# Kernel tuning notes

Hardware: AMD Instinct MI355X
Metric: run time of the kernel (lower is better)

## Reference

```python
import jax, jax.numpy as jnp
import numpy as np

NEG = -1e30  # stand-in for -inf on the H-attention diagonal (matches INF helper)


def _conv1x1(w, b, x):
    # w: [O, C], x: [B, C, H, W]
    return jnp.einsum('oc,bchw->bohw', w, x) + b[None, :, None, None]


def _cc_attn(q, k, v):
    """Criss-cross attention: q,k [B,Cq,H,W], v [B,C,H,W] -> [B,C,H,W]."""
    B, _, H, W = q.shape
    # column (H) energies: query at (h,w) attends to keys at (h', w)
    eH = jnp.einsum('bchw,bcjw->bhwj', q, k)  # [B,H,W,H]
    eye = jnp.eye(H, dtype=bool)[None, :, None, :]
    eH = jnp.where(eye, NEG, eH)  # mask h==h' (self counted once via W pass)
    # row (W) energies: query at (h,w) attends to keys at (h, w')
    eW = jnp.einsum('bchw,bchj->bhwj', q, k)  # [B,H,W,W]
    att = jax.nn.softmax(jnp.concatenate([eH, eW], axis=3), axis=3)  # [B,H,W,H+W]
    aH, aW = att[..., :H], att[..., H:]
    outH = jnp.einsum('bhwj,bcjw->bchw', aH, v)
    outW = jnp.einsum('bhwj,bchj->bchw', aW, v)
    return outH + outW


def setup_inputs() -> dict:
    key = jax.random.key(0)
    ks = jax.random.split(key, 14)
    B, C, H, W = 8, 256, 96, 96
    Cq = C // 8
    n = jax.random.normal
    return {
        'x': n(ks[0], (B, C, H, W), jnp.float32),
        'y': n(ks[1], (B, C, H, W), jnp.float32),
        'Wq': n(ks[2], (Cq, C), jnp.float32) * 0.05,
        'bq': n(ks[3], (Cq,), jnp.float32) * 0.05,
        'Wk': n(ks[4], (Cq, C), jnp.float32) * 0.05,
        'bk': n(ks[5], (Cq,), jnp.float32) * 0.05,
        'Wv': n(ks[6], (C, C), jnp.float32) * 0.05,
        'bv': n(ks[7], (C,), jnp.float32) * 0.05,
        'gamma1': n(ks[8], (1,), jnp.float32) * 0.1,
        'gamma2': n(ks[9], (1,), jnp.float32) * 0.1,
        'Wd': n(ks[10], (2 * C, 1, 3, 3), jnp.float32) * 0.1,  # depthwise, groups=2C
        'bd': n(ks[11], (2 * C,), jnp.float32) * 0.05,
        'Wp': n(ks[12], (C, 2 * C), jnp.float32) * 0.05,  # pointwise 1x1
        'bp': n(ks[13], (C,), jnp.float32) * 0.05,
    }


def reference(x, y, Wq, bq, Wk, bk, Wv, bv, gamma1, gamma2, Wd, bd, Wp, bp):
    qx = _conv1x1(Wq, bq, x)
    kx = _conv1x1(Wk, bk, x)
    vx = _conv1x1(Wv, bv, x)
    qy = _conv1x1(Wq, bq, y)
    ky = _conv1x1(Wk, bk, y)
    vy = _conv1x1(Wv, bv, y)
    # pass 1: attention weights from x, values from y
    out1 = gamma1[0] * _cc_attn(qx, kx, vy) + x
    # pass 2: attention weights from y, values from x
    out2 = gamma2[0] * _cc_attn(qy, ky, vx) + y
    z = jnp.concatenate([out1, out2], axis=1)  # [B, 2C, H, W]
    # depthwise 3x3 (groups = 2C), padding 1
    z = jax.lax.conv_general_dilated(
        z, Wd, window_strides=(1, 1), padding='SAME',
        feature_group_count=z.shape[1],
        dimension_numbers=('NCHW', 'OIHW', 'NCHW')) + bd[None, :, None, None]
    # pointwise 1x1 then LeakyReLU (torch default negative_slope=0.01)
    z = _conv1x1(Wp, bp, z)
    return jax.nn.leaky_relu(z, negative_slope=0.01)
```

## Files before the change

kernel.cpp:

```cpp
#include <hip/hip_runtime.h>
#include <hip/hip_bf16.h>

constexpr int kB  = 8;
constexpr int kC  = 256;
constexpr int kCq = 32;
constexpr int kH  = 96;
constexpr int kW  = 96;
constexpr int kP  = kH * kW;

using bf16x8 = __attribute__((ext_vector_type(8))) short;
using bf16x4 = __attribute__((ext_vector_type(4))) short;
using f32x4  = __attribute__((ext_vector_type(4))) float;

__device__ inline bf16x8 ld_lds8(const __hip_bfloat16* p) {
    bf16x4 lo = *(const bf16x4*)p;
    bf16x4 hi = *(const bf16x4*)(p + 4);
    return __builtin_shufflevector(lo, hi, 0, 1, 2, 3, 4, 5, 6, 7);
}

__global__ __launch_bounds__(256) void w_convert(
    const float* __restrict__ Wq, const float* __restrict__ Wk,
    const float* __restrict__ Wv,
    __hip_bfloat16* __restrict__ Wqkb, __hip_bfloat16* __restrict__ Wvb)
{
    const int i = blockIdx.x * 256 + threadIdx.x;
    if (i < 8192)       Wqkb[i] = __float2bfloat16(Wq[i]);
    else if (i < 16384) Wqkb[i] = __float2bfloat16(Wk[i - 8192]);
    else                Wvb[i - 16384] = __float2bfloat16(Wv[i - 16384]);
}

__global__ __launch_bounds__(256, 2) void qkv_mfma(
    const float* __restrict__ in_qk, const float* __restrict__ in_v,
    const __hip_bfloat16* __restrict__ Wqkb, const __hip_bfloat16* __restrict__ Wvb,
    const float* __restrict__ bq, const float* __restrict__ bk,
    const float* __restrict__ bv,
    __hip_bfloat16* __restrict__ Qbh, __hip_bfloat16* __restrict__ Qbl,
    __hip_bfloat16* __restrict__ Kbh, __hip_bfloat16* __restrict__ Kbl,
    __hip_bfloat16* __restrict__ Vpm, __hip_bfloat16* __restrict__ Vhw)
{
    __shared__ __align__(16) char smem[34816];
    __hip_bfloat16* sqb = (__hip_bfloat16*)smem;
    __hip_bfloat16* svb = sqb + 2 * 64 * 36;
    __hip_bfloat16* vt  = (__hip_bfloat16*)smem;

    const int b = blockIdx.y, t = threadIdx.x;
    const int wv = t >> 6, l = t & 63;
    const int n = l & 15, q = l >> 4;
    const int p0 = blockIdx.x * 64;
    const int p  = p0 + wv * 16 + n;
    const size_t bP = (size_t)b * kP;

    const float* __restrict__ xq = in_qk + (size_t)b * kC * kP + p0;
    const float* __restrict__ xv = in_v  + (size_t)b * kC * kP + p0;

    const int sc = t >> 4;
    const int sp = (t & 15) * 4;

    f32x4 acc[20];
#pragma unroll
    for (int i = 0; i < 20; i++) acc[i] = (f32x4)0.f;

    {
        float4 q0 = *(const float4*)&xq[(size_t)sc * kP + sp];
        float4 q1 = *(const float4*)&xq[(size_t)(16 + sc) * kP + sp];
        float4 v0 = *(const float4*)&xv[(size_t)sc * kP + sp];
        float4 v1 = *(const float4*)&xv[(size_t)(16 + sc) * kP + sp];
        float fq0[4] = { q0.x, q0.y, q0.z, q0.w };
        float fq1[4] = { q1.x, q1.y, q1.z, q1.w };
        float fv0[4] = { v0.x, v0.y, v0.z, v0.w };
        float fv1[4] = { v1.x, v1.y, v1.z, v1.w };
#pragma unroll
        for (int j = 0; j < 4; j++) {
            sqb[(sp + j) * 36 + sc]      = __float2bfloat16(fq0[j]);
            sqb[(sp + j) * 36 + 16 + sc] = __float2bfloat16(fq1[j]);
            svb[(sp + j) * 36 + sc]      = __float2bfloat16(fv0[j]);
            svb[(sp + j) * 36 + 16 + sc] = __float2bfloat16(fv1[j]);
        }
    }
    __syncthreads();

    int cur = 0;
    for (int kc = 0; kc < 8; kc++) {
        float4 nq0, nq1, nv0, nv1;
        if (kc < 7) {
            const size_t cb = (size_t)(kc + 1) * 32;
            nq0 = *(const float4*)&xq[(cb + sc) * kP + sp];
            nq1 = *(const float4*)&xq[(cb + 16 + sc) * kP + sp];
            nv0 = *(const float4*)&xv[(cb + sc) * kP + sp];
            nv1 = *(const float4*)&xv[(cb + 16 + sc) * kP + sp];
        }

        const int c0 = kc * 32 + q * 8;

        bf16x8 wq[4], wv2[16];
#pragma unroll
        for (int mt = 0; mt < 4; mt++)
            wq[mt] = *(const bf16x8*)(Wqkb + ((mt * 16 + n) << 8) + c0);
#pragma unroll
        for (int mt = 0; mt < 16; mt++)
            wv2[mt] = *(const bf16x8*)(Wvb + ((mt * 16 + n) << 8) + c0);

        const __hip_bfloat16* sqp = sqb + cur * 2304 + (wv * 16 + n) * 36 + q * 8;
        const __hip_bfloat16* svp = svb + cur * 2304 + (wv * 16 + n) * 36 + q * 8;
        bf16x8 bfq = ld_lds8(sqp);
        bf16x8 bfv = ld_lds8(svp);

#pragma unroll
        for (int mt = 0; mt < 4; mt++)
            acc[mt] = __builtin_amdgcn_mfma_f32_16x16x32_bf16(wq[mt], bfq, acc[mt], 0, 0, 0);
#pragma unroll
        for (int mt = 0; mt < 16; mt++)
            acc[4 + mt] = __builtin_amdgcn_mfma_f32_16x16x32_bf16(wv2[mt], bfv, acc[4 + mt], 0, 0, 0);

        if (kc < 7) {
            const int nb = cur ^ 1;
            __hip_bfloat16* dq = sqb + nb * 2304;
            __hip_bfloat16* dv = svb + nb * 2304;
            float fq0[4] = { nq0.x, nq0.y, nq0.z, nq0.w };
            float fq1[4] = { nq1.x, nq1.y, nq1.z, nq1.w };
            float fv0[4] = { nv0.x, nv0.y, nv0.z, nv0.w };
            float fv1[4] = { nv1.x, nv1.y, nv1.z, nv1.w };
#pragma unroll
            for (int j = 0; j < 4; j++) {
                dq[(sp + j) * 36 + sc]      = __float2bfloat16(fq0[j]);
                dq[(sp + j) * 36 + 16 + sc] = __float2bfloat16(fq1[j]);
                dv[(sp + j) * 36 + sc]      = __float2bfloat16(fv0[j]);
                dv[(sp + j) * 36 + 16 + sc] = __float2bfloat16(fv1[j]);
            }
        }
        __syncthreads();
        cur ^= 1;
    }

#pragma unroll
    for (int mt = 0; mt < 2; mt++) {
        float4 bias = *(const float4*)&bq[mt * 16 + q * 4];
        float vv[4] = { acc[mt][0] + bias.x, acc[mt][1] + bias.y,
                        acc[mt][2] + bias.z, acc[mt][3] + bias.w };
        union { ushort4 u; __hip_bfloat16 h[4]; } hi, lo;
#pragma unroll
        for (int r = 0; r < 4; r++) {
            __hip_bfloat16 h = __float2bfloat16(vv[r]);
            hi.h[r] = h;
            lo.h[r] = __float2bfloat16(vv[r] - __bfloat162float(h));
        }
        *(ushort4*)&Qbh[(bP + p) * kCq + mt * 16 + q * 4] = hi.u;
        *(ushort4*)&Qbl[(bP + p) * kCq + mt * 16 + q * 4] = lo.u;
    }
#pragma unroll
    for (int mt = 2; mt < 4; mt++) {
        float4 bias = *(const float4*)&bk[(mt - 2) * 16 + q * 4];
        float vv[4] = { acc[mt][0] + bias.x, acc[mt][1] + bias.y,
                        acc[mt][2] + bias.z, acc[mt][3] + bias.w };
        union { ushort4 u; __hip_bfloat16 h[4]; } hi, lo;
#pragma unroll
        for (int r = 0; r < 4; r++) {
            __hip_bfloat16 h = __float2bfloat16(vv[r]);
            hi.h[r] = h;
            lo.h[r] = __float2bfloat16(vv[r] - __bfloat162float(h));
        }
        *(ushort4*)&Kbh[(bP + p) * kCq + (mt - 2) * 16 + q * 4] = hi.u;
        *(ushort4*)&Kbl[(bP + p) * kCq + (mt - 2) * 16 + q * 4] = lo.u;
    }

#pragma unroll
    for (int mt = 0; mt < 16; mt++) {
        float4 bias = *(const float4*)&bv[mt * 16 + q * 4];
        float vv[4] = { acc[4 + mt][0] + bias.x, acc[4 + mt][1] + bias.y,
                        acc[4 + mt][2] + bias.z, acc[4 + mt][3] + bias.w };
        union { ushort4 u; __hip_bfloat16 h[4]; } pm;
#pragma unroll
        for (int r = 0; r < 4; r++) pm.h[r] = __float2bfloat16(vv[r]);
        *(ushort4*)&Vpm[(bP + p) * kC + mt * 16 + q * 4] = pm.u;
#pragma unroll
        for (int r = 0; r < 4; r++)
            vt[(mt * 16 + q * 4 + r) * 68 + wv * 16 + n] = pm.h[r];
    }
    __syncthreads();

    {
        __hip_bfloat16* dst = Vhw + ((size_t)b * kC + t) * kP + p0;
#pragma unroll
        for (int j = 0; j < 8; j++) {
            bf16x8 row = ld_lds8(&vt[t * 68 + j * 8]);
            *(bf16x8*)&dst[j * 8] = row;
        }
    }
}

__global__ __launch_bounds__(256) void cc_stats(
    const __hip_bfloat16* __restrict__ Qbh, const __hip_bfloat16* __restrict__ Qbl,
    const __hip_bfloat16* __restrict__ Kbh, const __hip_bfloat16* __restrict__ Kbl,
    float* __restrict__ Sm, float* __restrict__ Si)
{
    __shared__ __align__(16) __hip_bfloat16 QH[96][36], QLo[96][36];
    __shared__ __align__(16) __hip_bfloat16 KH[96][36], KLo[96][36];
    __shared__ __align__(16) float EL[96][97];
    const int w = blockIdx.x, b = blockIdx.y;
    const int t = threadIdx.x;
    const size_t bP = (size_t)b * kP;

    for (int idx = t; idx < 768; idx += 256) {
        int row = idx >> 3, ch = (idx & 7) * 4;
        size_t g = (bP + (size_t)row * kW + w) * kCq + ch;
        *(ushort4*)&QH[row][ch]  = *(const ushort4*)&Qbh[g];
        *(ushort4*)&QLo[row][ch] = *(const ushort4*)&Qbl[g];
        *(ushort4*)&KH[row][ch]  = *(const ushort4*)&Kbh[g];
        *(ushort4*)&KLo[row][ch] = *(const ushort4*)&Kbl[g];
    }
    __syncthreads();

    const int wv = t >> 6, l = t & 63, ln = l & 15, lq = l >> 4;
#pragma unroll
    for (int s = 0; s < 9; s++) {
        int tile = wv * 9 + s, it = tile / 6, jt = tile % 6;
        bf16x8 ah = ld_lds8(&QH[it * 16 + ln][lq * 8]);
        bf16x8 al = ld_lds8(&QLo[it * 16 + ln][lq * 8]);
        bf16x8 bh = ld_lds8(&KH[jt * 16 + ln][lq * 8]);
        bf16x8 bl = ld_lds8(&KLo[jt * 16 + ln][lq * 8]);
        f32x4 d = (f32x4)0.f;
        d = __builtin_amdgcn_mfma_f32_16x16x32_bf16(al, bh, d, 0, 0, 0);
        d = __builtin_amdgcn_mfma_f32_16x16x32_bf16(ah, bl, d, 0, 0, 0);
        d = __builtin_amdgcn_mfma_f32_16x16x32_bf16(ah, bh, d, 0, 0, 0);
#pragma unroll
        for (int r = 0; r < 4; r++)
            EL[it * 16 + lq * 4 + r][jt * 16 + ln] = d[r];
    }
    __syncthreads();

    const int sub = t & 7;
    for (int pi = t >> 3; pi < 96; pi += 32) {
        float ev[12];
        float mx = -3.0e38f;
#pragma unroll
        for (int k = 0; k < 12; k++) {
            int j = sub + 8 * k;
            float e = EL[pi][j];
            if (j == pi) e = -3.0e38f;
            ev[k] = e;
            mx = fmaxf(mx, e);
        }
#pragma unroll
        for (int k = 1; k < 8; k <<= 1) mx = fmaxf(mx, __shfl_xor(mx, k, 8));
        float ss = 0.f;
#pragma unroll
        for (int k = 0; k < 12; k++) ss += __expf(ev[k] - mx);
#pragma unroll
        for (int k = 1; k < 8; k <<= 1) ss += __shfl_xor(ss, k, 8);
        if (sub == 0) {
            Sm[bP + (size_t)pi * kW + w] = mx;
            Si[bP + (size_t)pi * kW + w] = ss;
        }
    }
}

__global__ __launch_bounds__(256) void cc_pass1(
    const __hip_bfloat16* __restrict__ Qbh, const __hip_bfloat16* __restrict__ Qbl,
    const __hip_bfloat16* __restrict__ Kbh, const __hip_bfloat16* __restrict__ Kbl,
    const __hip_bfloat16* __restrict__ Vhw,
    const float* __restrict__ res_in, const float* __restrict__ gamma_p,
    __hip_bfloat16* __restrict__ Zb, float* __restrict__ Sm, float* __restrict__ Si,
    int s_off)
{
    __shared__ __align__(16) __hip_bfloat16 QH[32][36], QLo[32][36];
    __shared__ __align__(16) __hip_bfloat16 KH[96][36], KLo[96][36];
    __shared__ __align__(16) float EL[32][97];
    __shared__ __align__(16) __hip_bfloat16 attL[32][100];
    __shared__ __align__(16) float rs[32][260];
    const int wt = blockIdx.x, h = blockIdx.y, b = blockIdx.z;
    const int w0 = wt * 32;
    const int t = threadIdx.x;
    const size_t bP = (size_t)b * kP;

    {
        int row = t >> 3, ch = (t & 7) * 4;
        size_t g = (bP + (size_t)h * kW + w0 + row) * kCq + ch;
        *(ushort4*)&QH[row][ch]  = *(const ushort4*)&Qbh[g];
        *(ushort4*)&QLo[row][ch] = *(const ushort4*)&Qbl[g];
    }
    for (int idx = t; idx < 768; idx += 256) {
        int row = idx >> 3, ch = (idx & 7) * 4;
        size_t g = (bP + (size_t)h * kW + row) * kCq + ch;
        *(ushort4*)&KH[row][ch]  = *(const ushort4*)&Kbh[g];
        *(ushort4*)&KLo[row][ch] = *(const ushort4*)&Kbl[g];
    }
    const float* __restrict__ res = res_in + (size_t)b * kC * kP + (size_t)h * kW + w0;
    {
        const int f4 = t & 7;
        int c2 = t >> 3;
#pragma unroll
        for (int it2 = 0; it2 < 8; it2++, c2 += 32) {
            float4 v = *(const float4*)&res[(size_t)c2 * kP + f4 * 4];
            rs[f4 * 4 + 0][c2] = v.x;
            rs[f4 * 4 + 1][c2] = v.y;
            rs[f4 * 4 + 2][c2] = v.z;
            rs[f4 * 4 + 3][c2] = v.w;
        }
    }
    __syncthreads();

    const int wv = t >> 6, l = t & 63, ln = l & 15, lq = l >> 4;
#pragma unroll
    for (int s = 0; s < 3; s++) {
        int tile = wv * 3 + s, it = tile / 6, jt = tile % 6;
        bf16x8 ah = ld_lds8(&QH[it * 16 + ln][lq * 8]);
        bf16x8 al = ld_lds8(&QLo[it * 16 + ln][lq * 8]);
        bf16x8 bh = ld_lds8(&KH[jt * 16 + ln][lq * 8]);
        bf16x8 bl = ld_lds8(&KLo[jt * 16 + ln][lq * 8]);
        f32x4 d = (f32x4)0.f;
        d = __builtin_amdgcn_mfma_f32_16x16x32_bf16(al, bh, d, 0, 0, 0);
        d = __builtin_amdgcn_mfma_f32_16x16x32_bf16(ah, bl, d, 0, 0, 0);
        d = __builtin_amdgcn_mfma_f32_16x16x32_bf16(ah, bh, d, 0, 0, 0);
#pragma unroll
        for (int r = 0; r < 4; r++)
            EL[it * 16 + lq * 4 + r][jt * 16 + ln] = d[r];
    }
    __syncthreads();

    {
        const int pi = t >> 3, sub = t & 7;
        size_t sidx = bP + (size_t)h * kW + w0 + pi;
        float mH = Sm[sidx], sH = Si[sidx];
        float ev[12];
        float mx = mH;
#pragma unroll
        for (int k = 0; k < 12; k++) {
            float e = EL[pi][sub + 8 * k];
            ev[k] = e;
            mx = fmaxf(mx, e);
        }
#pragma unroll
        for (int k = 1; k < 8; k <<= 1) mx = fmaxf(mx, __shfl_xor(mx, k, 8));
        float ss = 0.f;
#pragma unroll
        for (int k = 0; k < 12; k++) { float e = __expf(ev[k] - mx); ev[k] = e; ss += e; }
#pragma unroll
        for (int k = 1; k < 8; k <<= 1) ss += __shfl_xor(ss, k, 8);
        float stot = ss + sH * __expf(mH - mx);
        float inv = 1.0f / stot;
        if (sub == 0) { Sm[sidx] = mx; Si[sidx] = inv; }
#pragma unroll
        for (int k = 0; k < 12; k++)
            attL[pi][sub + 8 * k] = __float2bfloat16(ev[k] * inv);
    }
    __syncthreads();

    bf16x8 aF[2][3];
#pragma unroll
    for (int it = 0; it < 2; it++)
#pragma unroll
        for (int j3 = 0; j3 < 3; j3++)
            aF[it][j3] = ld_lds8(&attL[it * 16 + ln][j3 * 32 + lq * 8]);

    f32x4 acc[2][4];
#pragma unroll
    for (int it = 0; it < 2; it++)
#pragma unroll
        for (int c4 = 0; c4 < 4; c4++) acc[it][c4] = (f32x4)0.f;

#pragma unroll
    for (int c4 = 0; c4 < 4; c4++) {
        const int c = (wv * 4 + c4) * 16 + ln;
        const __hip_bfloat16* vr = Vhw + ((size_t)b * kC + c) * kP + (size_t)h * kW;
        bf16x8 bF0 = *(const bf16x8*)&vr[lq * 8];
        bf16x8 bF1 = *(const bf16x8*)&vr[32 + lq * 8];
        bf16x8 bF2 = *(const bf16x8*)&vr[64 + lq * 8];
#pragma unroll
        for (int it = 0; it < 2; it++) {
            acc[it][c4] = __builtin_amdgcn_mfma_f32_16x16x32_bf16(aF[it][0], bF0, acc[it][c4], 0, 0, 0);
            acc[it][c4] = __builtin_amdgcn_mfma_f32_16x16x32_bf16(aF[it][1], bF1, acc[it][c4], 0, 0, 0);
            acc[it][c4] = __builtin_amdgcn_mfma_f32_16x16x32_bf16(aF[it][2], bF2, acc[it][c4], 0, 0, 0);
        }
    }

    const float gamma = gamma_p[0];
#pragma unroll
    for (int c4 = 0; c4 < 4; c4++) {
        const int c = (wv * 4 + c4) * 16 + ln;
#pragma unroll
        for (int it = 0; it < 2; it++) {
#pragma unroll
            for (int r = 0; r < 4; r++) {
                int i = it * 16 + lq * 4 + r;
                float z = gamma * acc[it][c4][r] + rs[i][c];
                Zb[(bP + (size_t)h * kW + w0 + i) * 512 + s_off + c] = __float2bfloat16(z);
            }
        }
    }
}

__global__ __launch_bounds__(256) void cc_pass2(
    const __hip_bfloat16* __restrict__ Qbh, const __hip_bfloat16* __restrict__ Qbl,
    const __hip_bfloat16* __restrict__ Kbh, const __hip_bfloat16* __restrict__ Kbl,
    const __hip_bfloat16* __restrict__ Vpm,
    const float* __restrict__ gamma_p, __hip_bfloat16* __restrict__ Zb,
    const float* __restrict__ Sm, const float* __restrict__ Si, int s_off)
{
    __shared__ __align__(16) __hip_bfloat16 QH[32][36], QLo[32][36];
    __shared__ __align__(16) __hip_bfloat16 KH[96][36], KLo[96][36];
    __shared__ __align__(16) __hip_bfloat16 VL[96][260];
    __shared__ __align__(16) __hip_bfloat16 attL[32][100];
    const int ht = blockIdx.x, w = blockIdx.y, b = blockIdx.z;
    const int h0 = ht * 32;
    const int t = threadIdx.x;
    const size_t bP = (size_t)b * kP;

    {
        int row = t >> 3, ch = (t & 7) * 4;
        size_t g = (bP + (size_t)(h0 + row) * kW + w) * kCq + ch;
        *(ushort4*)&QH[row][ch]  = *(const ushort4*)&Qbh[g];
        *(ushort4*)&QLo[row][ch] = *(const ushort4*)&Qbl[g];
    }
    for (int idx = t; idx < 768; idx += 256) {
        int row = idx >> 3, ch = (idx & 7) * 4;
        size_t g = (bP + (size_t)row * kW + w) * kCq + ch;
        *(ushort4*)&KH[row][ch]  = *(const ushort4*)&Kbh[g];
        *(ushort4*)&KLo[row][ch] = *(const ushort4*)&Kbl[g];
    }
    for (int idx = t; idx < 96 * 32; idx += 256) {
        int j = idx >> 5, cg = (idx & 31) * 8;
        const ushort4* src = (const ushort4*)&Vpm[(bP + (size_t)j * kW + w) * kC + cg];
        ushort4 v0 = src[0], v1 = src[1];
        *(ushort4*)&VL[j][cg]     = v0;
        *(ushort4*)&VL[j][cg + 4] = v1;
    }
    __syncthreads();

    const int wv = t >> 6, l = t & 63, ln = l & 15, lq = l >> 4;
#pragma unroll
    for (int s = 0; s < 3; s++) {
        int tile = wv * 3 + s, it = tile / 6, jt = tile % 6;
        bf16x8 ah = ld_lds8(&QH[it * 16 + ln][lq * 8]);
        bf16x8 al = ld_lds8(&QLo[it * 16 + ln][lq * 8]);
        bf16x8 bh = ld_lds8(&KH[jt * 16 + ln][lq * 8]);
        bf16x8 bl = ld_lds8(&KLo[jt * 16 + ln][lq * 8]);
        f32x4 d = (f32x4)0.f;
        d = __builtin_amdgcn_mfma_f32_16x16x32_bf16(al, bh, d, 0, 0, 0);
        d = __builtin_amdgcn_mfma_f32_16x16x32_bf16(ah, bl, d, 0, 0, 0);
        d = __builtin_amdgcn_mfma_f32_16x16x32_bf16(ah, bh, d, 0, 0, 0);
        const int j = jt * 16 + ln;
#pragma unroll
        for (int r = 0; r < 4; r++) {
            int i = it * 16 + lq * 4 + r;
            size_t sidx = bP + (size_t)(h0 + i) * kW + w;
            float m = Sm[sidx], inv = Si[sidx];
            float a = (j == h0 + i) ? 0.f : __expf(d[r] - m) * inv;
            attL[i][j] = __float2bfloat16(a);
        }
    }
    __syncthreads();

    bf16x8 aF[2][3];
#pragma unroll
    for (int it = 0; it < 2; it++)
#pragma unroll
        for (int j3 = 0; j3 < 3; j3++)
            aF[it][j3] = ld_lds8(&attL[it * 16 + ln][j3 * 32 + lq * 8]);

    f32x4 acc[2][4];
#pragma unroll
    for (int it = 0; it < 2; it++)
#pragma unroll
        for (int c4 = 0; c4 < 4; c4++) acc[it][c4] = (f32x4)0.f;

#pragma unroll
    for (int c4 = 0; c4 < 4; c4++) {
        const int c = (wv * 4 + c4) * 16 + ln;
#pragma unroll
        for (int j3 = 0; j3 < 3; j3++) {
            union { bf16x8 v; __hip_bfloat16 h[8]; } bF;
#pragma unroll
            for (int jj = 0; jj < 8; jj++)
                bF.h[jj] = VL[j3 * 32 + lq * 8 + jj][c];
#pragma unroll
            for (int it = 0; it < 2; it++)
                acc[it][c4] = __builtin_amdgcn_mfma_f32_16x16x32_bf16(aF[it][j3], bF.v, acc[it][c4], 0, 0, 0);
        }
    }

    const float gamma = gamma_p[0];
#pragma unroll
    for (int c4 = 0; c4 < 4; c4++) {
        const int c = (wv * 4 + c4) * 16 + ln;
#pragma unroll
        for (int it = 0; it < 2; it++) {
#pragma unroll
            for (int r = 0; r < 4; r++) {
                int i = it * 16 + lq * 4 + r;
                size_t zi = (bP + (size_t)(h0 + i) * kW + w) * 512 + s_off + c;
                float old = __bfloat162float(Zb[zi]);
                Zb[zi] = __float2bfloat16(old + gamma * acc[it][c4][r]);
            }
        }
    }
}

__global__ __launch_bounds__(256) void wp_convert(
    const float* __restrict__ Wp, __hip_bfloat16* __restrict__ Wpb)
{
    const int i = blockIdx.x * 256 + threadIdx.x;
    Wpb[i] = __float2bfloat16(Wp[i]);
}

__global__ __launch_bounds__(256, 4) void dwpw(
    const __hip_bfloat16* __restrict__ Zb,
    const float* __restrict__ Wdw, const float* __restrict__ bd,
    const __hip_bfloat16* __restrict__ Wpb, const float* __restrict__ bp,
    float* __restrict__ out)
{
    __shared__ __align__(16) __hip_bfloat16 zs[16][520];

    const int wt = blockIdx.x, h = blockIdx.y, b = blockIdx.z;
    const int w0 = wt * 16;
    const int t = threadIdx.x;
    const size_t bP = (size_t)b * kP;

    const int l = t & 63, wv = t >> 6;
    const int lo16 = l & 15, q = l >> 4;

    const bf16x8* __restrict__ Bb[4];
#pragma unroll
    for (int nt = 0; nt < 4; nt++)
        Bb[nt] = (const bf16x8*)(Wpb + (size_t)(wv * 64 + nt * 16 + lo16) * 512);

    {
        float wd0[9], wd1[9];
#pragma unroll
        for (int k = 0; k < 9; k++) {
            wd0[k] = Wdw[(size_t)(2 * t) * 9 + k];
            wd1[k] = Wdw[(size_t)(2 * t + 1) * 9 + k];
        }
        const float b0 = bd[2 * t], b1 = bd[2 * t + 1];
        const uint* __restrict__ Zp = (const uint*)Zb + bP * 256 + t;
        const bool rvm = (h > 0), rvp = (h < kH - 1);

#pragma unroll
        for (int j0 = 0; j0 < 16; j0 += 8) {
            uint raw[10][3];
#pragma unroll
            for (int col = 0; col < 10; col++) {
                const int ww = w0 + j0 - 1 + col;
                const bool cv = (ww >= 0) && (ww < kW);
#pragma unroll
                for (int r = 0; r < 3; r++) {
                    const bool v = cv && (r == 1 || (r == 0 ? rvm : rvp));
                    raw[col][r] = v ? Zp[(size_t)((h + r - 1) * kW + ww) * 256] : 0u;
                }
            }
            float2 wfc[10][3];
#pragma unroll
            for (int col = 0; col < 10; col++)
#pragma unroll
                for (int r = 0; r < 3; r++) {
                    __hip_bfloat162 z2 = *(const __hip_bfloat162*)&raw[col][r];
                    wfc[col][r] = __bfloat1622float2(z2);
                }
#pragma unroll
            for (int j = 0; j < 8; j++) {
                float a0 = b0, a1 = b1;
#pragma unroll
                for (int r = 0; r < 3; r++) {
#pragma unroll
                    for (int dw = 0; dw < 3; dw++) {
                        const float2 z = wfc[j + dw][r];
                        const int k = r * 3 + dw;
                        a0 += wd0[k] * z.x;
                        a1 += wd1[k] * z.y;
                    }
                }
                __hip_bfloat162 pz;
                pz.x = __float2bfloat16(a0);
                pz.y = __float2bfloat16(a1);
                ((__hip_bfloat162*)&zs[j0 + j][0])[t] = pz;
            }
        }
    }

    bf16x8 wbuf[4][4];
#pragma unroll
    for (int kp = 0; kp < 4; kp++)
#pragma unroll
        for (int nt = 0; nt < 4; nt++)
            wbuf[kp][nt] = Bb[nt][kp * 4 + q];

    __syncthreads();

    f32x4 acc[4];
#pragma unroll
    for (int nt = 0; nt < 4; nt++) acc[nt] = (f32x4)0.f;

#pragma unroll
    for (int kc = 0; kc < 16; kc++) {
        const int s = kc & 3;
        bf16x8 a0 = ld_lds8(&zs[lo16][kc * 32 + q * 8]);
        bf16x8 wcur[4];
#pragma unroll
        for (int nt = 0; nt < 4; nt++) wcur[nt] = wbuf[s][nt];
        if (kc < 12) {
#pragma unroll
            for (int nt = 0; nt < 4; nt++)
                wbuf[s][nt] = Bb[nt][(kc + 4) * 4 + q];
        }
#pragma unroll
        for (int nt = 0; nt < 4; nt++)
            acc[nt] = __builtin_amdgcn_mfma_f32_16x16x32_bf16(a0, wcur[nt], acc[nt], 0, 0, 0);
    }

#pragma unroll
    for (int nt = 0; nt < 4; nt++) {
        const int ol = wv * 64 + nt * 16 + lo16;
        const float bias = bp[ol];
        float4 rv;
        float v0 = acc[nt][0] + bias; rv.x = v0 > 0.f ? v0 : 0.01f * v0;
        float v1 = acc[nt][1] + bias; rv.y = v1 > 0.f ? v1 : 0.01f * v1;
        float v2 = acc[nt][2] + bias; rv.z = v2 > 0.f ? v2 : 0.01f * v2;
        float v3 = acc[nt][3] + bias; rv.w = v3 > 0.f ? v3 : 0.01f * v3;
        *(float4*)&out[((size_t)b * 256 + ol) * kP + (size_t)h * kW + w0 + q * 4] = rv;
    }
}

extern "C" void kernel_launch(void* const* d_in, const int* in_sizes, int n_in,
                              void* d_out, int out_size, void* d_ws, size_t ws_size,
                              hipStream_t stream)
{
    const float* x   = (const float*)d_in[0];
    const float* y   = (const float*)d_in[1];
    const float* Wq  = (const float*)d_in[2];
    const float* bq  = (const float*)d_in[3];
    const float* Wk  = (const float*)d_in[4];
    const float* bk  = (const float*)d_in[5];
    const float* Wv  = (const float*)d_in[6];
    const float* bv  = (const float*)d_in[7];
    const float* g1  = (const float*)d_in[8];
    const float* g2  = (const float*)d_in[9];
    const float* Wdw = (const float*)d_in[10];
    const float* bd  = (const float*)d_in[11];
    const float* Wp  = (const float*)d_in[12];
    const float* bp  = (const float*)d_in[13];
    float* out = (float*)d_out;

    char* wsb = (char*)d_ws;
    __hip_bfloat16* Zb  = (__hip_bfloat16*)wsb;
    __hip_bfloat16* Qbh = (__hip_bfloat16*)(wsb + 75497472);
    __hip_bfloat16* Qbl = Qbh + 2359296;
    __hip_bfloat16* Kbh = (__hip_bfloat16*)(wsb + 84934656);
    __hip_bfloat16* Kbl = Kbh + 2359296;
    float* Sm = (float*)(wsb + 94371840);
    float* Si = (float*)(wsb + 94666752);
    __hip_bfloat16* Wqkb = (__hip_bfloat16*)Sm;
    __hip_bfloat16* Wvb  = ((__hip_bfloat16*)Sm) + 16384;
    __hip_bfloat16* Wpb  = (__hip_bfloat16*)(wsb + 75497472);
    __hip_bfloat16* Vpm  = (__hip_bfloat16*)d_out;
    __hip_bfloat16* Vhw  = Vpm + 18874368;

    hipLaunchKernelGGL(w_convert, dim3(320), dim3(256), 0, stream,
                       Wq, Wk, Wv, Wqkb, Wvb);
    hipLaunchKernelGGL(qkv_mfma, dim3(kP / 64, kB), dim3(256), 0, stream,
                       x, y, Wqkb, Wvb, bq, bk, bv, Qbh, Qbl, Kbh, Kbl, Vpm, Vhw);
    hipLaunchKernelGGL(cc_stats, dim3(kW, kB), dim3(256), 0, stream,
                       Qbh, Qbl, Kbh, Kbl, Sm, Si);
    hipLaunchKernelGGL(cc_pass1, dim3(kW / 32, kH, kB), dim3(256), 0, stream,
                       Qbh, Qbl, Kbh, Kbl, Vhw, x, g1, Zb, Sm, Si, 0);
    hipLaunchKernelGGL(cc_pass2, dim3(kH / 32, kW, kB), dim3(256), 0, stream,
                       Qbh, Qbl, Kbh, Kbl, Vpm, g1, Zb, Sm, Si, 0);
    hipLaunchKernelGGL(w_convert, dim3(320), dim3(256), 0, stream,
                       Wq, Wk, Wv, Wqkb, Wvb);
    hipLaunchKernelGGL(qkv_mfma, dim3(kP / 64, kB), dim3(256), 0, stream,
                       y, x, Wqkb, Wvb, bq, bk, bv, Qbh, Qbl, Kbh, Kbl, Vpm, Vhw);
    hipLaunchKernelGGL(cc_stats, dim3(kW, kB), dim3(256), 0, stream,
                       Qbh, Qbl, Kbh, Kbl, Sm, Si);
    hipLaunchKernelGGL(cc_pass1, dim3(kW / 32, kH, kB), dim3(256), 0, stream,
                       Qbh, Qbl, Kbh, Kbl, Vhw, y, g2, Zb, Sm, Si, 256);
    hipLaunchKernelGGL(cc_pass2, dim3(kH / 32, kW, kB), dim3(256), 0, stream,
                       Qbh, Qbl, Kbh, Kbl, Vpm, g2, Zb, Sm, Si, 256);
    hipLaunchKernelGGL(wp_convert, dim3(512), dim3(256), 0, stream, Wp, Wpb);
    hipLaunchKernelGGL(dwpw, dim3(kW / 16, kH, kB), dim3(256), 0, stream,
                       Zb, Wdw, bd, Wpb, bp, out);
}
```

Measured before the change: 829.5 us.

## Cut register pressure in depthwise+pointwise kernel to double occupancy

Result: slower. 919.1 us (+10.8%).

```diff
diff --git a/kernel.cpp b/kernel.cpp
--- a/kernel.cpp
+++ b/kernel.cpp
@@ -502,7 +502,7 @@
     Wpb[i] = __float2bfloat16(Wp[i]);
 }
 
-__global__ __launch_bounds__(256, 4) void dwpw(
+__global__ __launch_bounds__(256, 8) void dwpw(
     const __hip_bfloat16* __restrict__ Zb,
     const float* __restrict__ Wdw, const float* __restrict__ bd,
     const __hip_bfloat16* __restrict__ Wpb, const float* __restrict__ bp,
@@ -518,92 +518,82 @@
     const int l = t & 63, wv = t >> 6;
     const int lo16 = l & 15, q = l >> 4;
 
+    {
+        const float b0 = bd[2 * t], b1 = bd[2 * t + 1];
+        const uint* __restrict__ Zp = (const uint*)Zb + bP * 256 + t;
+        const float* __restrict__ wdp0 = Wdw + (size_t)(2 * t) * 9;
+        const float* __restrict__ wdp1 = Wdw + (size_t)(2 * t + 1) * 9;
+
+#pragma unroll
+        for (int j0 = 0; j0 < 16; j0 += 8) {
+            float a0[8], a1[8];
+#pragma unroll
+            for (int j = 0; j < 8; j++) { a0[j] = b0; a1[j] = b1; }
+
+#pragma unroll
+            for (int r = 0; r < 3; r++) {
+                const int hh = h + r - 1;
+                const int hcl = hh < 0 ? 0 : (hh > kH - 1 ? kH - 1 : hh);
+                const bool hv = (hh >= 0) && (hh < kH);
+
+                uint raw[10];
+#pragma unroll
+                for (int col = 0; col < 10; col++) {
+                    const int ww = w0 + j0 - 1 + col;
+                    const int wcl = ww < 0 ? 0 : (ww > kW - 1 ? kW - 1 : ww);
+                    const bool v = hv && (ww >= 0) && (ww < kW);
+                    uint val = Zp[(size_t)(hcl * kW + wcl) * 256];
+                    raw[col] = v ? val : 0u;
+                }
+                float w0r[3], w1r[3];
+#pragma unroll
+                for (int dw = 0; dw < 3; dw++) {
+                    w0r[dw] = wdp0[r * 3 + dw];
+                    w1r[dw] = wdp1[r * 3 + dw];
+                }
+                float2 f[10];
+#pragma unroll
+                for (int col = 0; col < 10; col++) {
+                    __hip_bfloat162 z2 = *(const __hip_bfloat162*)&raw[col];
+                    f[col] = __bfloat1622float2(z2);
+                }
+#pragma unroll
+                for (int j = 0; j < 8; j++) {
+#pragma unroll
+                    for (int dw = 0; dw < 3; dw++) {
+                        a0[j] += w0r[dw] * f[j + dw].x;
+                        a1[j] += w1r[dw] * f[j + dw].y;
+                    }
+                }
+            }
+
+#pragma unroll
+            for (int j = 0; j < 8; j++) {
+                __hip_bfloat162 pz;
+                pz.x = __float2bfloat16(a0[j]);
+                pz.y = __float2bfloat16(a1[j]);
+                ((__hip_bfloat162*)&zs[j0 + j][0])[t] = pz;
+            }
+        }
+    }
+    __syncthreads();
+
     const bf16x8* __restrict__ Bb[4];
 #pragma unroll
     for (int nt = 0; nt < 4; nt++)
         Bb[nt] = (const bf16x8*)(Wpb + (size_t)(wv * 64 + nt * 16 + lo16) * 512);
 
-    {
-        float wd0[9], wd1[9];
-#pragma unroll
-        for (int k = 0; k < 9; k++) {
-            wd0[k] = Wdw[(size_t)(2 * t) * 9 + k];
-            wd1[k] = Wdw[(size_t)(2 * t + 1) * 9 + k];
-        }
-        const float b0 = bd[2 * t], b1 = bd[2 * t + 1];
-        const uint* __restrict__ Zp = (const uint*)Zb + bP * 256 + t;
-        const bool rvm = (h > 0), rvp = (h < kH - 1);
-
-#pragma unroll
-        for (int j0 = 0; j0 < 16; j0 += 8) {
-            uint raw[10][3];
-#pragma unroll
-            for (int col = 0; col < 10; col++) {
-                const int ww = w0 + j0 - 1 + col;
-                const bool cv = (ww >= 0) && (ww < kW);
-#pragma unroll
-                for (int r = 0; r < 3; r++) {
-                    const bool v = cv && (r == 1 || (r == 0 ? rvm : rvp));
-                    raw[col][r] = v ? Zp[(size_t)((h + r - 1) * kW + ww) * 256] : 0u;
-                }
-            }
-            float2 wfc[10][3];
-#pragma unroll
-            for (int col = 0; col < 10; col++)
-#pragma unroll
-                for (int r = 0; r < 3; r++) {
-                    __hip_bfloat162 z2 = *(const __hip_bfloat162*)&raw[col][r];
-                    wfc[col][r] = __bfloat1622float2(z2);
-                }
-#pragma unroll
-            for (int j = 0; j < 8; j++) {
-                float a0 = b0, a1 = b1;
-#pragma unroll
-                for (int r = 0; r < 3; r++) {
-#pragma unroll
-                    for (int dw = 0; dw < 3; dw++) {
-                        const float2 z = wfc[j + dw][r];
-                        const int k = r * 3 + dw;
-                        a0 += wd0[k] * z.x;
-                        a1 += wd1[k] * z.y;
-                    }
-                }
-                __hip_bfloat162 pz;
-                pz.x = __float2bfloat16(a0);
-                pz.y = __float2bfloat16(a1);
-                ((__hip_bfloat162*)&zs[j0 + j][0])[t] = pz;
-            }
-        }
-    }
-
-    bf16x8 wbuf[4][4];
-#pragma unroll
-    for (int kp = 0; kp < 4; kp++)
-#pragma unroll
-        for (int nt = 0; nt < 4; nt++)
-            wbuf[kp][nt] = Bb[nt][kp * 4 + q];
-
-    __syncthreads();
-
     f32x4 acc[4];
 #pragma unroll
     for (int nt = 0; nt < 4; nt++) acc[nt] = (f32x4)0.f;
 
-#pragma unroll
     for (int kc = 0; kc < 16; kc++) {
-        const int s = kc & 3;
         bf16x8 a0 = ld_lds8(&zs[lo16][kc * 32 + q * 8]);
-        bf16x8 wcur[4];
-#pragma unroll
-        for (int nt = 0; nt < 4; nt++) wcur[nt] = wbuf[s][nt];
-        if (kc < 12) {
-#pragma unroll
-            for (int nt = 0; nt < 4; nt++)
-                wbuf[s][nt] = Bb[nt][(kc + 4) * 4 + q];
-        }
-#pragma unroll
-        for (int nt = 0; nt < 4; nt++)
-            acc[nt] = __builtin_amdgcn_mfma_f32_16x16x32_bf16(a0, wcur[nt], acc[nt], 0, 0, 0);
+#pragma unroll
+        for (int nt = 0; nt < 4; nt++) {
+            bf16x8 w = Bb[nt][kc * 4 + q];
+            acc[nt] = __builtin_amdgcn_mfma_f32_16x16x32_bf16(a0, w, acc[nt], 0, 0, 0);
+        }
     }
 
 #pragma unroll
```
